# Kernel optimization log

Hardware: AMD Instinct MI355X
Metric: run time of the kernel (lower is better)

Reference implementation:

```python
import jax, jax.numpy as jnp
import numpy as np

GAMMA = 0.99
LAM = 0.95
CLIP = 0.2
VALUE_COEFF = 0.5
ENTROPY_COEFF = 0.01
T = 500_000
S = 128
A = 16


def _mlp(x, W1, b1, W2, b2, W3, b3):
    h = jax.nn.relu(x @ W1 + b1)
    h = jax.nn.relu(h @ W2 + b2)
    return h @ W3 + b3


def setup_inputs() -> dict:
    key = jax.random.key(0)
    ks = jax.random.split(key, 12)
    states = jax.random.normal(ks[0], (T, S), dtype=jnp.float32)
    next_states = jax.random.normal(ks[1], (T, S), dtype=jnp.float32)
    rewards = jax.random.normal(ks[2], (T,), dtype=jnp.float32)
    dones = (jax.random.uniform(ks[3], (T,)) < 0.01).astype(jnp.float32)
    actions = jax.random.randint(ks[4], (T,), 0, A)
    # old log-probs of taken actions (valid log-probabilities)
    old_logp = jnp.log(jax.random.uniform(ks[5], (T,), minval=1e-3, maxval=1.0))

    def lin(k, fan_in, fan_out):
        lim = 1.0 / np.sqrt(fan_in)
        return jax.random.uniform(k, (fan_in, fan_out), minval=-lim, maxval=lim, dtype=jnp.float32)

    return {
        'states': states, 'next_states': next_states, 'rewards': rewards,
        'dones': dones, 'actions': actions, 'old_logp': old_logp,
        'aW1': lin(ks[6], S, 64), 'ab1': jnp.zeros((64,), jnp.float32),
        'aW2': lin(ks[7], 64, 64), 'ab2': jnp.zeros((64,), jnp.float32),
        'aW3': lin(ks[8], 64, A), 'ab3': jnp.zeros((A,), jnp.float32),
        'cW1': lin(ks[9], S, 64), 'cb1': jnp.zeros((64,), jnp.float32),
        'cW2': lin(ks[10], 64, 64), 'cb2': jnp.zeros((64,), jnp.float32),
        'cW3': lin(ks[11], 64, 1), 'cb3': jnp.zeros((1,), jnp.float32),
    }


def reference(states, next_states, rewards, dones, actions, old_logp,
              aW1, ab1, aW2, ab2, aW3, ab3,
              cW1, cb1, cW2, cb2, cW3, cb3):
    # ---- critic values and TD deltas ----
    values = _mlp(states, cW1, cb1, cW2, cb2, cW3, cb3)[:, 0]        # [T]
    next_values = _mlp(next_states, cW1, cb1, cW2, cb2, cW3, cb3)[:, 0]
    not_done = 1.0 - dones
    deltas = rewards + GAMMA * next_values * not_done - values       # [T]

    # ---- GAE: reverse-time linear recurrence a_t = c_t * a_{t+1} + d_t ----
    coef = GAMMA * LAM * not_done

    def step(carry, cd):
        c, d = cd
        a = c * carry + d
        return a, a

    _, advantages = jax.lax.scan(step, jnp.float32(0.0), (coef, deltas), reverse=True)
    returns = advantages + values
    adv_n = (advantages - advantages.mean()) / (jnp.std(advantages, ddof=1) + 1e-8)

    # ---- actor: clipped surrogate ----
    probs = jax.nn.softmax(_mlp(states, aW1, ab1, aW2, ab2, aW3, ab3), axis=-1)  # [T, A]
    logp = jnp.log(jnp.take_along_axis(probs, actions[:, None], axis=1))[:, 0]   # [T]
    ratios = jnp.exp(logp - old_logp)
    surr1 = ratios * adv_n
    surr2 = jnp.clip(ratios, 1.0 - CLIP, 1.0 + CLIP) * adv_n
    actor_loss = -jnp.minimum(surr1, surr2).mean()

    # ---- critic MSE loss ----
    critic_loss = jnp.mean((values - returns) ** 2)

    # ---- entropy bonus ----
    entropy_loss = jnp.mean(-jnp.sum(probs * jnp.log(probs + 1e-8), axis=-1))

    total_loss = actor_loss + VALUE_COEFF * critic_loss - ENTROPY_COEFF * entropy_loss
    return jnp.stack([total_loss, actor_loss, critic_loss, entropy_loss])
```

## Files before the change

kernel.cpp:

```cpp
#include <hip/hip_runtime.h>

#define T_N 500000
#define NTILE 31250
#define NCHUNK 4096
#define CHUNKL 128
#define NPART 1024

typedef __attribute__((ext_vector_type(8))) short short8v;
typedef __attribute__((ext_vector_type(4))) float float4v;

__device__ __forceinline__ short f2bf(float f) {
    union { float f; unsigned u; } v; v.f = f;
    unsigned r = v.u + 0x7FFFu + ((v.u >> 16) & 1u);
    return (short)(r >> 16);
}

#define FC1 0
#define FA1 16
#define FC2 32
#define FA2 40
#define FA3 48
#define NFRAG 50

__global__ __launch_bounds__(64) void k_pack(
    const float* __restrict__ cW1, const float* __restrict__ aW1,
    const float* __restrict__ cW2, const float* __restrict__ aW2,
    const float* __restrict__ aW3, short8v* __restrict__ packed)
{
    const int f = blockIdx.x, l = threadIdx.x;
    const int g = l >> 4, col = l & 15;
    const float* W; int s, c, ncol;
    if (f < FA1)      { W = cW1; s = f >> 2;         c = f & 3;         ncol = 64; }
    else if (f < FC2) { W = aW1; s = (f - FA1) >> 2; c = (f - FA1) & 3; ncol = 64; }
    else if (f < FA2) { W = cW2; s = (f - FC2) >> 2; c = (f - FC2) & 3; ncol = 64; }
    else if (f < FA3) { W = aW2; s = (f - FA2) >> 2; c = (f - FA2) & 3; ncol = 64; }
    else              { W = aW3; s = f - FA3;        c = 0;             ncol = 16; }
    short8v frag;
    #pragma unroll
    for (int j = 0; j < 8; ++j) {
        int k = s * 32 + g * 8 + j;
        frag[j] = f2bf(W[k * ncol + c * 16 + col]);
    }
    packed[f * 64 + l] = frag;
}

__global__ __launch_bounds__(256) void k_mlp(
    const float* __restrict__ states, const float* __restrict__ next_states,
    const float* __restrict__ rewards, const float* __restrict__ dones,
    const int* __restrict__ actions, const float* __restrict__ old_logp,
    const short8v* __restrict__ pk,
    const float* __restrict__ cb1, const float* __restrict__ ab1,
    const float* __restrict__ cb2, const float* __restrict__ ab2,
    const float* __restrict__ ab3,
    const float* __restrict__ cW3, const float* __restrict__ cb3,
    float* __restrict__ delta_o, float* __restrict__ coef_o,
    float* __restrict__ ratio_o, float* __restrict__ ent_o)
{
    __shared__ __align__(16) short hlds[4][16][72];
    const int wv = threadIdx.x >> 6, l = threadIdx.x & 63;
    const int g = l >> 4, q = l & 15;
    const long long tile = (long long)blockIdx.x * 4 + wv;
    if (tile >= NTILE) return;
    const long long r0 = tile * 16;
    short (*h)[72] = hlds[wv];

    float4v accC[4], accA[4];
    #pragma unroll
    for (int c = 0; c < 4; ++c) {
        float b = cb1[c * 16 + q];  accC[c] = (float4v){b, b, b, b};
        float b2 = ab1[c * 16 + q]; accA[c] = (float4v){b2, b2, b2, b2};
    }
    {
        const float* xs = states + (r0 + q) * 128;
        #pragma unroll
        for (int s = 0; s < 4; ++s) {
            float4 xa = *reinterpret_cast<const float4*>(xs + s * 32 + g * 8);
            float4 xb = *reinterpret_cast<const float4*>(xs + s * 32 + g * 8 + 4);
            short8v af;
            af[0] = f2bf(xa.x); af[1] = f2bf(xa.y); af[2] = f2bf(xa.z); af[3] = f2bf(xa.w);
            af[4] = f2bf(xb.x); af[5] = f2bf(xb.y); af[6] = f2bf(xb.z); af[7] = f2bf(xb.w);
            #pragma unroll
            for (int c = 0; c < 4; ++c) {
                accC[c] = __builtin_amdgcn_mfma_f32_16x16x32_bf16(af, pk[(FC1 + s * 4 + c) * 64 + l], accC[c], 0, 0, 0);
                accA[c] = __builtin_amdgcn_mfma_f32_16x16x32_bf16(af, pk[(FA1 + s * 4 + c) * 64 + l], accA[c], 0, 0, 0);
            }
        }
    }

    #pragma unroll
    for (int c = 0; c < 4; ++c)
        #pragma unroll
        for (int r = 0; r < 4; ++r)
            h[g * 4 + r][c * 16 + q] = f2bf(fmaxf(accC[c][r], 0.f));
    float4v acc2[4];
    #pragma unroll
    for (int c = 0; c < 4; ++c) { float b = cb2[c * 16 + q]; acc2[c] = (float4v){b, b, b, b}; }
    #pragma unroll
    for (int s = 0; s < 2; ++s) {
        short8v a2 = *reinterpret_cast<const short8v*>(&h[q][s * 32 + g * 8]);
        #pragma unroll
        for (int c = 0; c < 4; ++c)
            acc2[c] = __builtin_amdgcn_mfma_f32_16x16x32_bf16(a2, pk[(FC2 + s * 4 + c) * 64 + l], acc2[c], 0, 0, 0);
    }
    float vr[4] = {0.f, 0.f, 0.f, 0.f};
    #pragma unroll
    for (int c = 0; c < 4; ++c) {
        float w = cW3[c * 16 + q];
        #pragma unroll
        for (int r = 0; r < 4; ++r) vr[r] = fmaf(fmaxf(acc2[c][r], 0.f), w, vr[r]);
    }
    #pragma unroll
    for (int o = 1; o < 16; o <<= 1)
        #pragma unroll
        for (int r = 0; r < 4; ++r) vr[r] += __shfl_xor(vr[r], o);
    const float cb3v = cb3[0];
    float v[4];
    #pragma unroll
    for (int r = 0; r < 4; ++r) v[r] = vr[r] + cb3v;

    #pragma unroll
    for (int c = 0; c < 4; ++c)
        #pragma unroll
        for (int r = 0; r < 4; ++r)
            h[g * 4 + r][c * 16 + q] = f2bf(fmaxf(accA[c][r], 0.f));
    float4v acc2a[4];
    #pragma unroll
    for (int c = 0; c < 4; ++c) { float b = ab2[c * 16 + q]; acc2a[c] = (float4v){b, b, b, b}; }
    #pragma unroll
    for (int s = 0; s < 2; ++s) {
        short8v a2 = *reinterpret_cast<const short8v*>(&h[q][s * 32 + g * 8]);
        #pragma unroll
        for (int c = 0; c < 4; ++c)
            acc2a[c] = __builtin_amdgcn_mfma_f32_16x16x32_bf16(a2, pk[(FA2 + s * 4 + c) * 64 + l], acc2a[c], 0, 0, 0);
    }
    #pragma unroll
    for (int c = 0; c < 4; ++c)
        #pragma unroll
        for (int r = 0; r < 4; ++r)
            h[g * 4 + r][c * 16 + q] = f2bf(fmaxf(acc2a[c][r], 0.f));
    const float b3 = ab3[q];
    float4v acc3 = (float4v){b3, b3, b3, b3};
    #pragma unroll
    for (int s = 0; s < 2; ++s) {
        short8v a3 = *reinterpret_cast<const short8v*>(&h[q][s * 32 + g * 8]);
        acc3 = __builtin_amdgcn_mfma_f32_16x16x32_bf16(a3, pk[(FA3 + s) * 64 + l], acc3, 0, 0, 0);
    }
    float lg[4], mx[4], pe[4], se[4], entv[4], sl[4], logp[4];
    #pragma unroll
    for (int r = 0; r < 4; ++r) { lg[r] = acc3[r]; mx[r] = lg[r]; }
    #pragma unroll
    for (int o = 1; o < 16; o <<= 1)
        #pragma unroll
        for (int r = 0; r < 4; ++r) mx[r] = fmaxf(mx[r], __shfl_xor(mx[r], o));
    #pragma unroll
    for (int r = 0; r < 4; ++r) { pe[r] = expf(lg[r] - mx[r]); se[r] = pe[r]; }
    #pragma unroll
    for (int o = 1; o < 16; o <<= 1)
        #pragma unroll
        for (int r = 0; r < 4; ++r) se[r] += __shfl_xor(se[r], o);
    #pragma unroll
    for (int r = 0; r < 4; ++r) { float pr = pe[r] / se[r]; entv[r] = -pr * logf(pr + 1e-8f); }
    #pragma unroll
    for (int o = 1; o < 16; o <<= 1)
        #pragma unroll
        for (int r = 0; r < 4; ++r) entv[r] += __shfl_xor(entv[r], o);
    const int4 av = *reinterpret_cast<const int4*>(&actions[r0 + g * 4]);
    const int act[4] = {av.x, av.y, av.z, av.w};
    #pragma unroll
    for (int r = 0; r < 4; ++r) sl[r] = (q == act[r]) ? lg[r] : -3.0e38f;
    #pragma unroll
    for (int o = 1; o < 16; o <<= 1)
        #pragma unroll
        for (int r = 0; r < 4; ++r) sl[r] = fmaxf(sl[r], __shfl_xor(sl[r], o));
    #pragma unroll
    for (int r = 0; r < 4; ++r) logp[r] = sl[r] - mx[r] - logf(se[r]);

    float4v accN[4];
    #pragma unroll
    for (int c = 0; c < 4; ++c) { float b = cb1[c * 16 + q]; accN[c] = (float4v){b, b, b, b}; }
    {
        const float* xn = next_states + (r0 + q) * 128;
        #pragma unroll
        for (int s = 0; s < 4; ++s) {
            float4 xa = *reinterpret_cast<const float4*>(xn + s * 32 + g * 8);
            float4 xb = *reinterpret_cast<const float4*>(xn + s * 32 + g * 8 + 4);
            short8v af;
            af[0] = f2bf(xa.x); af[1] = f2bf(xa.y); af[2] = f2bf(xa.z); af[3] = f2bf(xa.w);
            af[4] = f2bf(xb.x); af[5] = f2bf(xb.y); af[6] = f2bf(xb.z); af[7] = f2bf(xb.w);
            #pragma unroll
            for (int c = 0; c < 4; ++c)
                accN[c] = __builtin_amdgcn_mfma_f32_16x16x32_bf16(af, pk[(FC1 + s * 4 + c) * 64 + l], accN[c], 0, 0, 0);
        }
    }
    #pragma unroll
    for (int c = 0; c < 4; ++c)
        #pragma unroll
        for (int r = 0; r < 4; ++r)
            h[g * 4 + r][c * 16 + q] = f2bf(fmaxf(accN[c][r], 0.f));
    float4v acc2n[4];
    #pragma unroll
    for (int c = 0; c < 4; ++c) { float b = cb2[c * 16 + q]; acc2n[c] = (float4v){b, b, b, b}; }
    #pragma unroll
    for (int s = 0; s < 2; ++s) {
        short8v a2 = *reinterpret_cast<const short8v*>(&h[q][s * 32 + g * 8]);
        #pragma unroll
        for (int c = 0; c < 4; ++c)
            acc2n[c] = __builtin_amdgcn_mfma_f32_16x16x32_bf16(a2, pk[(FC2 + s * 4 + c) * 64 + l], acc2n[c], 0, 0, 0);
    }
    float nr[4] = {0.f, 0.f, 0.f, 0.f};
    #pragma unroll
    for (int c = 0; c < 4; ++c) {
        float w = cW3[c * 16 + q];
        #pragma unroll
        for (int r = 0; r < 4; ++r) nr[r] = fmaf(fmaxf(acc2n[c][r], 0.f), w, nr[r]);
    }
    #pragma unroll
    for (int o = 1; o < 16; o <<= 1)
        #pragma unroll
        for (int r = 0; r < 4; ++r) nr[r] += __shfl_xor(nr[r], o);
    float nv[4];
    #pragma unroll
    for (int r = 0; r < 4; ++r) nv[r] = nr[r] + cb3v;

    if (q == 0) {
        const long long rb = r0 + g * 4;
        const float4 rw = *reinterpret_cast<const float4*>(&rewards[rb]);
        const float4 dn = *reinterpret_cast<const float4*>(&dones[rb]);
        const float4 ol = *reinterpret_cast<const float4*>(&old_logp[rb]);
        const float rwv[4] = {rw.x, rw.y, rw.z, rw.w};
        const float dnv[4] = {dn.x, dn.y, dn.z, dn.w};
        const float olv[4] = {ol.x, ol.y, ol.z, ol.w};
        float dl[4], cf[4], rt[4];
        const float GL = (float)(0.99 * 0.95);
        #pragma unroll
        for (int r = 0; r < 4; ++r) {
            float nd = 1.f - dnv[r];
            dl[r] = fmaf(0.99f * nd, nv[r], rwv[r]) - v[r];
            cf[r] = GL * nd;
            rt[r] = expf(logp[r] - olv[r]);
        }
        float4 t;
        t.x = dl[0]; t.y = dl[1]; t.z = dl[2]; t.w = dl[3];
        *reinterpret_cast<float4*>(&delta_o[rb]) = t;
        t.x = cf[0]; t.y = cf[1]; t.z = cf[2]; t.w = cf[3];
        *reinterpret_cast<float4*>(&coef_o[rb]) = t;
        t.x = rt[0]; t.y = rt[1]; t.z = rt[2]; t.w = rt[3];
        *reinterpret_cast<float4*>(&ratio_o[rb]) = t;
        t.x = entv[0]; t.y = entv[1]; t.z = entv[2]; t.w = entv[3];
        *reinterpret_cast<float4*>(&ent_o[rb]) = t;
    }
}

__global__ __launch_bounds__(256) void k_gae_chunk(
    const float* __restrict__ coef, const float* __restrict__ delta,
    float* __restrict__ P, float* __restrict__ Q)
{
    const int c = blockIdx.x * 256 + threadIdx.x;
    const long long lo = (long long)c * CHUNKL;
    float p = 1.f, a = 0.f;
    if (lo < T_N) {
        const int n = (int)((T_N - lo < CHUNKL) ? (T_N - lo) : CHUNKL);
        for (int j = (n >> 2) - 1; j >= 0; --j) {
            float4 cfv = *reinterpret_cast<const float4*>(&coef[lo + 4 * j]);
            float4 dlv = *reinterpret_cast<const float4*>(&delta[lo + 4 * j]);
            a = fmaf(cfv.w, a, dlv.w);
            a = fmaf(cfv.z, a, dlv.z);
            a = fmaf(cfv.y, a, dlv.y);
            a = fmaf(cfv.x, a, dlv.x);
            p *= cfv.x * cfv.y * cfv.z * cfv.w;
        }
    }
    P[c] = p; Q[c] = a;
}

__global__ __launch_bounds__(1024) void k_gae_scan(
    const float* __restrict__ P, const float* __restrict__ Q,
    float* __restrict__ carry)
{
    __shared__ float sp[1024], sq[1024];
    const int t = threadIdx.x, b = t * 4;
    float p = P[b + 3], q = Q[b + 3];
    #pragma unroll
    for (int c = 2; c >= 0; --c) {
        float pc = P[b + c], qc = Q[b + c];
        q = fmaf(pc, q, qc);
        p = pc * p;
    }
    sp[t] = p; sq[t] = q;
    __syncthreads();
    for (int d = 1; d < 1024; d <<= 1) {
        float pp = sp[t], qq = sq[t];
        float p2 = 1.f, q2 = 0.f;
        const bool has = (t + d) < 1024;
        if (has) { p2 = sp[t + d]; q2 = sq[t + d]; }
        __syncthreads();
        if (has) { sp[t] = pp * p2; sq[t] = fmaf(pp, q2, qq); }
        __syncthreads();
    }
    float x = (t + 1 < 1024) ? sq[t + 1] : 0.f;
    #pragma unroll
    for (int c = 3; c >= 0; --c) {
        carry[b + c] = x;
        x = fmaf(P[b + c], x, Q[b + c]);
    }
}

__global__ __launch_bounds__(256) void k_gae_apply(
    const float* __restrict__ coef, const float* __restrict__ delta,
    const float* __restrict__ carry, float* __restrict__ adv,
    float* __restrict__ part)
{
    const int c = blockIdx.x * 256 + threadIdx.x;
    const long long lo = (long long)c * CHUNKL;
    float s = 0.f, s2 = 0.f;
    if (lo < T_N) {
        const int n = (int)((T_N - lo < CHUNKL) ? (T_N - lo) : CHUNKL);
        float a = carry[c];
        for (int j = (n >> 2) - 1; j >= 0; --j) {
            float4 cfv = *reinterpret_cast<const float4*>(&coef[lo + 4 * j]);
            float4 dlv = *reinterpret_cast<const float4*>(&delta[lo + 4 * j]);
            float a3 = fmaf(cfv.w, a, dlv.w);
            float a2v = fmaf(cfv.z, a3, dlv.z);
            float a1 = fmaf(cfv.y, a2v, dlv.y);
            float a0 = fmaf(cfv.x, a1, dlv.x);
            float4 o; o.x = a0; o.y = a1; o.z = a2v; o.w = a3;
            *reinterpret_cast<float4*>(&adv[lo + 4 * j]) = o;
            a = a0;
            s += a0 + a1 + a2v + a3;
            s2 += a0 * a0 + a1 * a1 + a2v * a2v + a3 * a3;
        }
    }
    #pragma unroll
    for (int o = 32; o > 0; o >>= 1) { s += __shfl_down(s, o); s2 += __shfl_down(s2, o); }
    __shared__ float l0[4], l1[4];
    const int wv = threadIdx.x >> 6, ln = threadIdx.x & 63;
    if (ln == 0) { l0[wv] = s; l1[wv] = s2; }
    __syncthreads();
    if (threadIdx.x == 0) {
        part[blockIdx.x * 2]     = l0[0] + l0[1] + l0[2] + l0[3];
        part[blockIdx.x * 2 + 1] = l1[0] + l1[1] + l1[2] + l1[3];
    }
}

__global__ __launch_bounds__(256) void k_actor(
    const float* __restrict__ adv, const float* __restrict__ ratio,
    const float* __restrict__ ent, const float* __restrict__ part,
    float* __restrict__ part4)
{
    __shared__ float st[2];
    if (threadIdx.x == 0) {
        float S = 0.f, S2 = 0.f;
        #pragma unroll
        for (int i = 0; i < 16; ++i) { S += part[2 * i]; S2 += part[2 * i + 1]; }
        const float Tf = (float)T_N;
        float mean = S / Tf;
        float var = (S2 - S * S / Tf) / (Tf - 1.f);
        st[0] = mean;
        st[1] = 1.f / (sqrtf(fmaxf(var, 0.f)) + 1e-8f);
    }
    __syncthreads();
    const float mean = st[0], isd = st[1];
    float sm = 0.f, se = 0.f;
    for (long long i = (long long)blockIdx.x * 256 + threadIdx.x; i < T_N;
         i += (long long)gridDim.x * 256) {
        float an = (adv[i] - mean) * isd;
        float rt = ratio[i];
        float s1 = rt * an;
        float s2v = fminf(fmaxf(rt, 0.8f), 1.2f) * an;
        sm += fminf(s1, s2v);
        se += ent[i];
    }
    #pragma unroll
    for (int o = 32; o > 0; o >>= 1) { sm += __shfl_down(sm, o); se += __shfl_down(se, o); }
    __shared__ float l0[4], l1[4];
    const int wv = threadIdx.x >> 6, ln = threadIdx.x & 63;
    if (ln == 0) { l0[wv] = sm; l1[wv] = se; }
    __syncthreads();
    if (threadIdx.x == 0) {
        part4[blockIdx.x * 2]     = l0[0] + l0[1] + l0[2] + l0[3];
        part4[blockIdx.x * 2 + 1] = l1[0] + l1[1] + l1[2] + l1[3];
    }
}

__global__ __launch_bounds__(1024) void k_final(
    const float* __restrict__ part4, const float* __restrict__ part,
    float* __restrict__ out)
{
    const int t = threadIdx.x;
    float sm = part4[t * 2], se = part4[t * 2 + 1];
    #pragma unroll
    for (int o = 32; o > 0; o >>= 1) { sm += __shfl_down(sm, o); se += __shfl_down(se, o); }
    __shared__ float l0[16], l1[16];
    const int wv = t >> 6, ln = t & 63;
    if (ln == 0) { l0[wv] = sm; l1[wv] = se; }
    __syncthreads();
    if (t == 0) {
        float SM = 0.f, SE = 0.f;
        #pragma unroll
        for (int i = 0; i < 16; ++i) { SM += l0[i]; SE += l1[i]; }
        float S2 = 0.f;
        #pragma unroll
        for (int i = 0; i < 16; ++i) S2 += part[2 * i + 1];
        const float Tf = (float)T_N;
        float actor_loss = -SM / Tf;
        float ent_loss = SE / Tf;
        float critic_loss = S2 / Tf;
        float total = actor_loss + 0.5f * critic_loss - 0.01f * ent_loss;
        out[0] = total; out[1] = actor_loss; out[2] = critic_loss; out[3] = ent_loss;
    }
}

extern "C" void kernel_launch(void* const* d_in, const int* in_sizes, int n_in,
                              void* d_out, int out_size, void* d_ws, size_t ws_size,
                              hipStream_t stream) {
    (void)in_sizes; (void)n_in; (void)out_size; (void)ws_size;
    const float* states      = (const float*)d_in[0];
    const float* next_states = (const float*)d_in[1];
    const float* rewards     = (const float*)d_in[2];
    const float* dones       = (const float*)d_in[3];
    const int*   actions     = (const int*)d_in[4];
    const float* old_logp    = (const float*)d_in[5];
    const float* aW1 = (const float*)d_in[6];  const float* ab1 = (const float*)d_in[7];
    const float* aW2 = (const float*)d_in[8];  const float* ab2 = (const float*)d_in[9];
    const float* aW3 = (const float*)d_in[10]; const float* ab3 = (const float*)d_in[11];
    const float* cW1 = (const float*)d_in[12]; const float* cb1 = (const float*)d_in[13];
    const float* cW2 = (const float*)d_in[14]; const float* cb2 = (const float*)d_in[15];
    const float* cW3 = (const float*)d_in[16]; const float* cb3 = (const float*)d_in[17];
    float* out = (float*)d_out;

    float* ws = (float*)d_ws;
    float* delta = ws;
    float* coef  = ws + 1 * (size_t)T_N;
    float* ratio = ws + 2 * (size_t)T_N;
    float* entb  = ws + 3 * (size_t)T_N;
    float* adv   = ws + 4 * (size_t)T_N;
    float* P     = ws + 5 * (size_t)T_N;
    float* Q     = P + NCHUNK;
    float* carry = Q + NCHUNK;
    float* part  = carry + NCHUNK;
    float* part4 = part + 32;
    short8v* packed = (short8v*)(part4 + 2048);

    k_pack<<<NFRAG, 64, 0, stream>>>(cW1, aW1, cW2, aW2, aW3, packed);
    k_mlp<<<(NTILE + 3) / 4, 256, 0, stream>>>(
        states, next_states, rewards, dones, actions, old_logp, packed,
        cb1, ab1, cb2, ab2, ab3, cW3, cb3, delta, coef, ratio, entb);
    k_gae_chunk<<<NCHUNK / 256, 256, 0, stream>>>(coef, delta, P, Q);
    k_gae_scan<<<1, 1024, 0, stream>>>(P, Q, carry);
    k_gae_apply<<<NCHUNK / 256, 256, 0, stream>>>(coef, delta, carry, adv, part);
    k_actor<<<NPART, 256, 0, stream>>>(adv, ratio, entb, part, part4);
    k_final<<<1, 1024, 0, stream>>>(part4, part, out);
}
```

Measured before the change: 224.6 us.

## Restructure MLP kernel: preload both inputs, interleave critic passes, cheaper softmax math

```diff
diff --git a/kernel.cpp b/kernel.cpp
--- a/kernel.cpp
+++ b/kernel.cpp
@@ -1,4 +1,5 @@
 #include <hip/hip_runtime.h>
+#include <hip/hip_bf16.h>
 
 #define T_N 500000
 #define NTILE 31250
@@ -10,9 +11,15 @@
 typedef __attribute__((ext_vector_type(4))) float float4v;
 
 __device__ __forceinline__ short f2bf(float f) {
-    union { float f; unsigned u; } v; v.f = f;
-    unsigned r = v.u + 0x7FFFu + ((v.u >> 16) & 1u);
-    return (short)(r >> 16);
+    __hip_bfloat16 b = __float2bfloat16(f);
+    return *reinterpret_cast<short*>(&b);
+}
+
+__device__ __forceinline__ short8v cvt8(const float4 a, const float4 b) {
+    short8v r;
+    r[0] = f2bf(a.x); r[1] = f2bf(a.y); r[2] = f2bf(a.z); r[3] = f2bf(a.w);
+    r[4] = f2bf(b.x); r[5] = f2bf(b.y); r[6] = f2bf(b.z); r[7] = f2bf(b.w);
+    return r;
 }
 
 #define FC1 0
@@ -44,7 +51,15 @@
     packed[f * 64 + l] = frag;
 }
 
-__global__ __launch_bounds__(256) void k_mlp(
+__device__ __forceinline__ void store_h(short (*hb)[68], const float4v* acc, int g, int q) {
+    #pragma unroll
+    for (int c = 0; c < 4; ++c)
+        #pragma unroll
+        for (int r = 0; r < 4; ++r)
+            hb[g * 4 + r][c * 16 + q] = f2bf(fmaxf(acc[c][r], 0.f));
+}
+
+__global__ __launch_bounds__(256, 4) void k_mlp(
     const float* __restrict__ states, const float* __restrict__ next_states,
     const float* __restrict__ rewards, const float* __restrict__ dones,
     const int* __restrict__ actions, const float* __restrict__ old_logp,
@@ -56,171 +71,152 @@
     float* __restrict__ delta_o, float* __restrict__ coef_o,
     float* __restrict__ ratio_o, float* __restrict__ ent_o)
 {
-    __shared__ __align__(16) short hlds[4][16][72];
+    __shared__ __align__(16) short hlds[4][2][16][68];
     const int wv = threadIdx.x >> 6, l = threadIdx.x & 63;
     const int g = l >> 4, q = l & 15;
-    const long long tile = (long long)blockIdx.x * 4 + wv;
+    const int tile = blockIdx.x * 4 + wv;
     if (tile >= NTILE) return;
-    const long long r0 = tile * 16;
-    short (*h)[72] = hlds[wv];
-
-    float4v accC[4], accA[4];
+    const long long r0 = (long long)tile * 16;
+    short (*h0)[68] = hlds[wv][0];
+    short (*h1)[68] = hlds[wv][1];
+
+    const float* xs = states + (r0 + q) * 128 + g * 8;
+    const float* xn = next_states + (r0 + q) * 128 + g * 8;
+    float4 rs[8], rn[8];
+    #pragma unroll
+    for (int s = 0; s < 4; ++s) {
+        rs[2 * s]     = *reinterpret_cast<const float4*>(xs + s * 32);
+        rs[2 * s + 1] = *reinterpret_cast<const float4*>(xs + s * 32 + 4);
+    }
+    #pragma unroll
+    for (int s = 0; s < 4; ++s) {
+        rn[2 * s]     = *reinterpret_cast<const float4*>(xn + s * 32);
+        rn[2 * s + 1] = *reinterpret_cast<const float4*>(xn + s * 32 + 4);
+    }
+    short8v sa[4], na[4];
+    #pragma unroll
+    for (int s = 0; s < 4; ++s) sa[s] = cvt8(rs[2 * s], rs[2 * s + 1]);
+    #pragma unroll
+    for (int s = 0; s < 4; ++s) na[s] = cvt8(rn[2 * s], rn[2 * s + 1]);
+
+    float4v accC[4], accN[4];
     #pragma unroll
     for (int c = 0; c < 4; ++c) {
-        float b = cb1[c * 16 + q];  accC[c] = (float4v){b, b, b, b};
-        float b2 = ab1[c * 16 + q]; accA[c] = (float4v){b2, b2, b2, b2};
-    }
-    {
-        const float* xs = states + (r0 + q) * 128;
-        #pragma unroll
-        for (int s = 0; s < 4; ++s) {
-            float4 xa = *reinterpret_cast<const float4*>(xs + s * 32 + g * 8);
-            float4 xb = *reinterpret_cast<const float4*>(xs + s * 32 + g * 8 + 4);
-            short8v af;
-            af[0] = f2bf(xa.x); af[1] = f2bf(xa.y); af[2] = f2bf(xa.z); af[3] = f2bf(xa.w);
-            af[4] = f2bf(xb.x); af[5] = f2bf(xb.y); af[6] = f2bf(xb.z); af[7] = f2bf(xb.w);
-            #pragma unroll
-            for (int c = 0; c < 4; ++c) {
-                accC[c] = __builtin_amdgcn_mfma_f32_16x16x32_bf16(af, pk[(FC1 + s * 4 + c) * 64 + l], accC[c], 0, 0, 0);
-                accA[c] = __builtin_amdgcn_mfma_f32_16x16x32_bf16(af, pk[(FA1 + s * 4 + c) * 64 + l], accA[c], 0, 0, 0);
-            }
-        }
-    }
-
-    #pragma unroll
-    for (int c = 0; c < 4; ++c)
-        #pragma unroll
-        for (int r = 0; r < 4; ++r)
-            h[g * 4 + r][c * 16 + q] = f2bf(fmaxf(accC[c][r], 0.f));
-    float4v acc2[4];
-    #pragma unroll
-    for (int c = 0; c < 4; ++c) { float b = cb2[c * 16 + q]; acc2[c] = (float4v){b, b, b, b}; }
+        float b = cb1[c * 16 + q];
+        accC[c] = (float4v){b, b, b, b};
+        accN[c] = accC[c];
+    }
+    #pragma unroll
+    for (int s = 0; s < 4; ++s) {
+        #pragma unroll
+        for (int c = 0; c < 4; ++c) {
+            short8v w = pk[(FC1 + s * 4 + c) * 64 + l];
+            accC[c] = __builtin_amdgcn_mfma_f32_16x16x32_bf16(sa[s], w, accC[c], 0, 0, 0);
+            accN[c] = __builtin_amdgcn_mfma_f32_16x16x32_bf16(na[s], w, accN[c], 0, 0, 0);
+        }
+    }
+    store_h(h0, accC, g, q);
+    store_h(h1, accN, g, q);
+
+    float4v c2C[4], c2N[4];
+    #pragma unroll
+    for (int c = 0; c < 4; ++c) {
+        float b = cb2[c * 16 + q];
+        c2C[c] = (float4v){b, b, b, b};
+        c2N[c] = c2C[c];
+    }
     #pragma unroll
     for (int s = 0; s < 2; ++s) {
-        short8v a2 = *reinterpret_cast<const short8v*>(&h[q][s * 32 + g * 8]);
+        short8v aC = *reinterpret_cast<const short8v*>(&h0[q][s * 32 + g * 8]);
+        short8v aN = *reinterpret_cast<const short8v*>(&h1[q][s * 32 + g * 8]);
+        #pragma unroll
+        for (int c = 0; c < 4; ++c) {
+            short8v w = pk[(FC2 + s * 4 + c) * 64 + l];
+            c2C[c] = __builtin_amdgcn_mfma_f32_16x16x32_bf16(aC, w, c2C[c], 0, 0, 0);
+            c2N[c] = __builtin_amdgcn_mfma_f32_16x16x32_bf16(aN, w, c2N[c], 0, 0, 0);
+        }
+    }
+    float vr[4] = {0.f, 0.f, 0.f, 0.f}, nr[4] = {0.f, 0.f, 0.f, 0.f};
+    #pragma unroll
+    for (int c = 0; c < 4; ++c) {
+        float w3 = cW3[c * 16 + q];
+        #pragma unroll
+        for (int r = 0; r < 4; ++r) {
+            vr[r] = fmaf(fmaxf(c2C[c][r], 0.f), w3, vr[r]);
+            nr[r] = fmaf(fmaxf(c2N[c][r], 0.f), w3, nr[r]);
+        }
+    }
+    #pragma unroll
+    for (int o = 1; o < 16; o <<= 1)
+        #pragma unroll
+        for (int r = 0; r < 4; ++r) {
+            vr[r] += __shfl_xor(vr[r], o);
+            nr[r] += __shfl_xor(nr[r], o);
+        }
+    const float cb3v = cb3[0];
+    float v[4], nv[4];
+    #pragma unroll
+    for (int r = 0; r < 4; ++r) { v[r] = vr[r] + cb3v; nv[r] = nr[r] + cb3v; }
+
+    float4v aA[4];
+    #pragma unroll
+    for (int c = 0; c < 4; ++c) { float b = ab1[c * 16 + q]; aA[c] = (float4v){b, b, b, b}; }
+    #pragma unroll
+    for (int s = 0; s < 4; ++s)
         #pragma unroll
         for (int c = 0; c < 4; ++c)
-            acc2[c] = __builtin_amdgcn_mfma_f32_16x16x32_bf16(a2, pk[(FC2 + s * 4 + c) * 64 + l], acc2[c], 0, 0, 0);
-    }
-    float vr[4] = {0.f, 0.f, 0.f, 0.f};
-    #pragma unroll
-    for (int c = 0; c < 4; ++c) {
-        float w = cW3[c * 16 + q];
-        #pragma unroll
-        for (int r = 0; r < 4; ++r) vr[r] = fmaf(fmaxf(acc2[c][r], 0.f), w, vr[r]);
-    }
+            aA[c] = __builtin_amdgcn_mfma_f32_16x16x32_bf16(sa[s], pk[(FA1 + s * 4 + c) * 64 + l], aA[c], 0, 0, 0);
+    store_h(h0, aA, g, q);
+
+    float4v a2[4];
+    #pragma unroll
+    for (int c = 0; c < 4; ++c) { float b = ab2[c * 16 + q]; a2[c] = (float4v){b, b, b, b}; }
+    #pragma unroll
+    for (int s = 0; s < 2; ++s) {
+        short8v aa = *reinterpret_cast<const short8v*>(&h0[q][s * 32 + g * 8]);
+        #pragma unroll
+        for (int c = 0; c < 4; ++c)
+            a2[c] = __builtin_amdgcn_mfma_f32_16x16x32_bf16(aa, pk[(FA2 + s * 4 + c) * 64 + l], a2[c], 0, 0, 0);
+    }
+    store_h(h1, a2, g, q);
+
+    const float b3 = ab3[q];
+    float4v a3 = (float4v){b3, b3, b3, b3};
+    #pragma unroll
+    for (int s = 0; s < 2; ++s) {
+        short8v aa = *reinterpret_cast<const short8v*>(&h1[q][s * 32 + g * 8]);
+        a3 = __builtin_amdgcn_mfma_f32_16x16x32_bf16(aa, pk[(FA3 + s) * 64 + l], a3, 0, 0, 0);
+    }
+
+    float lg[4], mx[4], pe[4], se[4], tt[4], ent[4], logp[4];
+    #pragma unroll
+    for (int r = 0; r < 4; ++r) { lg[r] = a3[r]; mx[r] = lg[r]; }
     #pragma unroll
     for (int o = 1; o < 16; o <<= 1)
         #pragma unroll
-        for (int r = 0; r < 4; ++r) vr[r] += __shfl_xor(vr[r], o);
-    const float cb3v = cb3[0];
-    float v[4];
-    #pragma unroll
-    for (int r = 0; r < 4; ++r) v[r] = vr[r] + cb3v;
-
-    #pragma unroll
-    for (int c = 0; c < 4; ++c)
-        #pragma unroll
-        for (int r = 0; r < 4; ++r)
-            h[g * 4 + r][c * 16 + q] = f2bf(fmaxf(accA[c][r], 0.f));
-    float4v acc2a[4];
-    #pragma unroll
-    for (int c = 0; c < 4; ++c) { float b = ab2[c * 16 + q]; acc2a[c] = (float4v){b, b, b, b}; }
-    #pragma unroll
-    for (int s = 0; s < 2; ++s) {
-        short8v a2 = *reinterpret_cast<const short8v*>(&h[q][s * 32 + g * 8]);
-        #pragma unroll
-        for (int c = 0; c < 4; ++c)
-            acc2a[c] = __builtin_amdgcn_mfma_f32_16x16x32_bf16(a2, pk[(FA2 + s * 4 + c) * 64 + l], acc2a[c], 0, 0, 0);
-    }
-    #pragma unroll
-    for (int c = 0; c < 4; ++c)
-        #pragma unroll
-        for (int r = 0; r < 4; ++r)
-            h[g * 4 + r][c * 16 + q] = f2bf(fmaxf(acc2a[c][r], 0.f));
-    const float b3 = ab3[q];
-    float4v acc3 = (float4v){b3, b3, b3, b3};
-    #pragma unroll
-    for (int s = 0; s < 2; ++s) {
-        short8v a3 = *reinterpret_cast<const short8v*>(&h[q][s * 32 + g * 8]);
-        acc3 = __builtin_amdgcn_mfma_f32_16x16x32_bf16(a3, pk[(FA3 + s) * 64 + l], acc3, 0, 0, 0);
-    }
-    float lg[4], mx[4], pe[4], se[4], entv[4], sl[4], logp[4];
-    #pragma unroll
-    for (int r = 0; r < 4; ++r) { lg[r] = acc3[r]; mx[r] = lg[r]; }
+        for (int r = 0; r < 4; ++r) mx[r] = fmaxf(mx[r], __shfl_xor(mx[r], o));
+    #pragma unroll
+    for (int r = 0; r < 4; ++r) {
+        pe[r] = __expf(lg[r] - mx[r]);
+        se[r] = pe[r];
+        tt[r] = pe[r] * lg[r];
+    }
     #pragma unroll
     for (int o = 1; o < 16; o <<= 1)
         #pragma unroll
-        for (int r = 0; r < 4; ++r) mx[r] = fmaxf(mx[r], __shfl_xor(mx[r], o));
-    #pragma unroll
-    for (int r = 0; r < 4; ++r) { pe[r] = expf(lg[r] - mx[r]); se[r] = pe[r]; }
-    #pragma unroll
-    for (int o = 1; o < 16; o <<= 1)
-        #pragma unroll
-        for (int r = 0; r < 4; ++r) se[r] += __shfl_xor(se[r], o);
-    #pragma unroll
-    for (int r = 0; r < 4; ++r) { float pr = pe[r] / se[r]; entv[r] = -pr * logf(pr + 1e-8f); }
-    #pragma unroll
-    for (int o = 1; o < 16; o <<= 1)
-        #pragma unroll
-        for (int r = 0; r < 4; ++r) entv[r] += __shfl_xor(entv[r], o);
+        for (int r = 0; r < 4; ++r) {
+            se[r] += __shfl_xor(se[r], o);
+            tt[r] += __shfl_xor(tt[r], o);
+        }
     const int4 av = *reinterpret_cast<const int4*>(&actions[r0 + g * 4]);
     const int act[4] = {av.x, av.y, av.z, av.w};
     #pragma unroll
-    for (int r = 0; r < 4; ++r) sl[r] = (q == act[r]) ? lg[r] : -3.0e38f;
-    #pragma unroll
-    for (int o = 1; o < 16; o <<= 1)
-        #pragma unroll
-        for (int r = 0; r < 4; ++r) sl[r] = fmaxf(sl[r], __shfl_xor(sl[r], o));
-    #pragma unroll
-    for (int r = 0; r < 4; ++r) logp[r] = sl[r] - mx[r] - logf(se[r]);
-
-    float4v accN[4];
-    #pragma unroll
-    for (int c = 0; c < 4; ++c) { float b = cb1[c * 16 + q]; accN[c] = (float4v){b, b, b, b}; }
-    {
-        const float* xn = next_states + (r0 + q) * 128;
-        #pragma unroll
-        for (int s = 0; s < 4; ++s) {
-            float4 xa = *reinterpret_cast<const float4*>(xn + s * 32 + g * 8);
-            float4 xb = *reinterpret_cast<const float4*>(xn + s * 32 + g * 8 + 4);
-            short8v af;
-            af[0] = f2bf(xa.x); af[1] = f2bf(xa.y); af[2] = f2bf(xa.z); af[3] = f2bf(xa.w);
-            af[4] = f2bf(xb.x); af[5] = f2bf(xb.y); af[6] = f2bf(xb.z); af[7] = f2bf(xb.w);
-            #pragma unroll
-            for (int c = 0; c < 4; ++c)
-                accN[c] = __builtin_amdgcn_mfma_f32_16x16x32_bf16(af, pk[(FC1 + s * 4 + c) * 64 + l], accN[c], 0, 0, 0);
-        }
-    }
-    #pragma unroll
-    for (int c = 0; c < 4; ++c)
-        #pragma unroll
-        for (int r = 0; r < 4; ++r)
-            h[g * 4 + r][c * 16 + q] = f2bf(fmaxf(accN[c][r], 0.f));
-    float4v acc2n[4];
-    #pragma unroll
-    for (int c = 0; c < 4; ++c) { float b = cb2[c * 16 + q]; acc2n[c] = (float4v){b, b, b, b}; }
-    #pragma unroll
-    for (int s = 0; s < 2; ++s) {
-        short8v a2 = *reinterpret_cast<const short8v*>(&h[q][s * 32 + g * 8]);
-        #pragma unroll
-        for (int c = 0; c < 4; ++c)
-            acc2n[c] = __builtin_amdgcn_mfma_f32_16x16x32_bf16(a2, pk[(FC2 + s * 4 + c) * 64 + l], acc2n[c], 0, 0, 0);
-    }
-    float nr[4] = {0.f, 0.f, 0.f, 0.f};
-    #pragma unroll
-    for (int c = 0; c < 4; ++c) {
-        float w = cW3[c * 16 + q];
-        #pragma unroll
-        for (int r = 0; r < 4; ++r) nr[r] = fmaf(fmaxf(acc2n[c][r], 0.f), w, nr[r]);
-    }
-    #pragma unroll
-    for (int o = 1; o < 16; o <<= 1)
-        #pragma unroll
-        for (int r = 0; r < 4; ++r) nr[r] += __shfl_xor(nr[r], o);
-    float nv[4];
-    #pragma unroll
-    for (int r = 0; r < 4; ++r) nv[r] = nr[r] + cb3v;
+    for (int r = 0; r < 4; ++r) {
+        float ls = __logf(se[r]);
+        ent[r] = mx[r] + ls - tt[r] / se[r];
+        float sel = __shfl(lg[r], (l & 48) | act[r]);
+        logp[r] = sel - mx[r] - ls;
+    }
 
     if (q == 0) {
         const long long rb = r0 + g * 4;
@@ -230,14 +226,14 @@
         const float rwv[4] = {rw.x, rw.y, rw.z, rw.w};
         const float dnv[4] = {dn.x, dn.y, dn.z, dn.w};
         const float olv[4] = {ol.x, ol.y, ol.z, ol.w};
+        const float GL = 0.99f * 0.95f;
         float dl[4], cf[4], rt[4];
-        const float GL = (float)(0.99 * 0.95);
         #pragma unroll
         for (int r = 0; r < 4; ++r) {
             float nd = 1.f - dnv[r];
             dl[r] = fmaf(0.99f * nd, nv[r], rwv[r]) - v[r];
             cf[r] = GL * nd;
-            rt[r] = expf(logp[r] - olv[r]);
+            rt[r] = __expf(logp[r] - olv[r]);
         }
         float4 t;
         t.x = dl[0]; t.y = dl[1]; t.z = dl[2]; t.w = dl[3];
@@ -246,7 +242,7 @@
         *reinterpret_cast<float4*>(&coef_o[rb]) = t;
         t.x = rt[0]; t.y = rt[1]; t.z = rt[2]; t.w = rt[3];
         *reinterpret_cast<float4*>(&ratio_o[rb]) = t;
-        t.x = entv[0]; t.y = entv[1]; t.z = entv[2]; t.w = entv[3];
+        t.x = ent[0]; t.y = ent[1]; t.z = ent[2]; t.w = ent[3];
         *reinterpret_cast<float4*>(&ent_o[rb]) = t;
     }
 }
```

After: 214.7 us. 1.05x faster.
